# Kernel optimization log

Measured on AMD Instinct MI355X. Metric: run time of the kernel, lower is better.

The kernel has to match this reference:

```python
import jax, jax.numpy as jnp
import numpy as np

N = 50000      # nodes
E = 400000     # edges
G = 128        # graphs in batch
D_NODE = 64
EDGE_DIM = 72
HEADS = 4
H0, H1, H2 = 128, 128, 64
NC = 2
NEG = 0.2      # GATConv leaky_relu negative_slope default
D1 = H2 + EDGE_DIM - 1  # ffn input dim = 135


def _p(k, shape, s=0.1):
    return jax.random.normal(k, shape, dtype=jnp.float32) * s


def setup_inputs() -> dict:
    key = jax.random.key(0)
    ks = jax.random.split(key, 24)
    x = jax.random.normal(ks[0], (N, D_NODE), dtype=jnp.float32)
    edge_index = jax.random.randint(ks[1], (2, E), 0, N)
    edge_attr = jax.random.uniform(ks[2], (E, EDGE_DIM), dtype=jnp.float32)
    batch = jnp.sort(jax.random.randint(ks[3], (N,), 0, G))
    return dict(
        x=x, edge_index=edge_index, edge_attr=edge_attr, batch=batch,
        # GATConv layer 1: in=D_NODE, out=H0, heads=HEADS, concat
        W1=_p(ks[4], (D_NODE, HEADS * H0)), We1=_p(ks[5], (EDGE_DIM, HEADS * H0)),
        as1=_p(ks[6], (HEADS, H0)), ad1=_p(ks[7], (HEADS, H0)), ae1=_p(ks[8], (HEADS, H0)),
        b1=jnp.zeros((HEADS * H0,), jnp.float32),
        # GATConv layer 2: in=HEADS*H0, out=H1, heads=HEADS, concat
        W2=_p(ks[9], (HEADS * H0, HEADS * H1)), We2=_p(ks[10], (EDGE_DIM, HEADS * H1)),
        as2=_p(ks[11], (HEADS, H1)), ad2=_p(ks[12], (HEADS, H1)), ae2=_p(ks[13], (HEADS, H1)),
        b2=jnp.zeros((HEADS * H1,), jnp.float32),
        # GATConv layer 3: in=HEADS*H1, out=H2, heads=1, concat=False
        W3=_p(ks[14], (HEADS * H1, H2)), We3=_p(ks[15], (EDGE_DIM, H2)),
        as3=_p(ks[16], (1, H2)), ad3=_p(ks[17], (1, H2)), ae3=_p(ks[18], (1, H2)),
        b3=jnp.zeros((H2,), jnp.float32),
        # ffn: Linear(135 -> 67), ReLU, Linear(67 -> 2), Softmax
        Wf1=_p(ks[19], (D1, D1 // 2)), bf1=jnp.zeros((D1 // 2,), jnp.float32),
        Wf2=_p(ks[20], (D1 // 2, NC)), bf2=jnp.zeros((NC,), jnp.float32),
    )


def _seg_softmax(s, seg, n):
    # numerically-stable softmax over segments (per-destination neighborhoods)
    m = jax.ops.segment_max(s, seg, num_segments=n)
    m = jnp.where(jnp.isfinite(m), m, 0.0)
    e = jnp.exp(s - m[seg])
    z = jax.ops.segment_sum(e, seg, num_segments=n)
    return e / (z[seg] + 1e-16)


def _gat(x, src, dst, eattr, W, We, a_s, a_d, a_e, b, heads, oc, concat):
    # PyG GATConv with edge_dim: shared src/dst projection, edge feats only in attention
    n = x.shape[0]
    xs = (x @ W).reshape(n, heads, oc)            # [N,H,C]
    ee = (eattr @ We).reshape(-1, heads, oc)      # [Ea,H,C]
    alpha = (xs * a_s).sum(-1)[src] + (xs * a_d).sum(-1)[dst] + (ee * a_e).sum(-1)
    alpha = jax.nn.leaky_relu(alpha, NEG)         # [Ea,H]
    alpha = _seg_softmax(alpha, dst, n)
    out = jax.ops.segment_sum(xs[src] * alpha[:, :, None], dst, num_segments=n)
    out = out.reshape(n, heads * oc) if concat else out.mean(axis=1)
    return out + b


def reference(x, edge_index, edge_attr, batch,
              W1, We1, as1, ad1, ae1, b1,
              W2, We2, as2, ad2, ae2, b2,
              W3, We3, as3, ad3, ae3, b3,
              Wf1, bf1, Wf2, bf2):
    src, dst = edge_index[0], edge_index[1]
    n = x.shape[0]
    # --- 1-gram feature vector: scatter-add edge_attr[:, :-1] by graph of src ---
    eb = batch[src]
    og = jax.ops.segment_sum(edge_attr[:, :-1], eb, num_segments=G)   # [G, EDGE_DIM-1]
    og = og / jnp.maximum(jnp.linalg.norm(og, axis=1, keepdims=True), 1e-12)
    # --- add self loops, edge_attr fill_value='mean' (mean over incoming edges) ---
    ones_e = jnp.ones((src.shape[0],), x.dtype)
    deg = jax.ops.segment_sum(ones_e, dst, num_segments=n)
    loop_attr = jax.ops.segment_sum(edge_attr, dst, num_segments=n) / jnp.maximum(deg, 1.0)[:, None]
    nodes = jnp.arange(n)
    src_a = jnp.concatenate([src, nodes])
    dst_a = jnp.concatenate([dst, nodes])
    ea = jnp.concatenate([edge_attr, loop_attr], axis=0)
    # --- GAT stack with ReLU activations ---
    h = jax.nn.relu(_gat(x, src_a, dst_a, ea, W1, We1, as1, ad1, ae1, b1, HEADS, H0, True))
    h = jax.nn.relu(_gat(h, src_a, dst_a, ea, W2, We2, as2, ad2, ae2, b2, HEADS, H1, True))
    h = jax.nn.relu(_gat(h, src_a, dst_a, ea, W3, We3, as3, ad3, ae3, b3, 1, H2, False))
    # --- global mean pool over graphs ---
    cnt = jax.ops.segment_sum(jnp.ones((n,), x.dtype), batch, num_segments=G)
    pooled = jax.ops.segment_sum(h, batch, num_segments=G) / jnp.maximum(cnt, 1.0)[:, None]
    # --- concat + ffn (dropout p=0 in eval) + softmax ---
    z = jnp.concatenate([pooled, og], axis=1)                         # [G, 135]
    z = jax.nn.relu(z @ Wf1 + bf1)
    return jax.nn.softmax(z @ Wf2 + bf2, axis=1)
```

## Files before the change

kernel.cpp:

```cpp
#include <hip/hip_runtime.h>

#define NNODES 50000
#define NEDGES 400000
#define NEA    450000
#define NG     128
#define DEGCAP 96
#define OGW    72
#define NCH    49
#define PREPN  1128328
#define PREPB  4408
#define EDGEB  1563
#define OGB    (NG*16)

typedef unsigned short u16;
typedef unsigned int   u32;
typedef __attribute__((ext_vector_type(8))) short short8v;
typedef __attribute__((ext_vector_type(4))) float f32x4;

static inline int ceil_div(int a, int b){ return (a + b - 1)/b; }

__device__ __forceinline__ u16 f2bf(float f){
  u32 u = __builtin_bit_cast(u32, f);
  u = (u + 0x7fffu + ((u >> 16) & 1u)) >> 16;
  return (u16)u;
}
__device__ __forceinline__ float bfLO(u32 q){ return __builtin_bit_cast(float, q << 16); }
__device__ __forceinline__ float bfHI(u32 q){ return __builtin_bit_cast(float, q & 0xffff0000u); }
__device__ __forceinline__ void gload_lds16(const u16* g, u16* l){
  __builtin_amdgcn_global_load_lds((const __attribute__((address_space(1))) void*)g,
                                   (__attribute__((address_space(3))) void*)l, 16, 0, 0);
}

__global__ void k_prep_deg(const float* __restrict__ x, u16* __restrict__ xb,
                       const float* __restrict__ W1, u16* __restrict__ Wt1,
                       const float* __restrict__ W2, u16* __restrict__ Wt2,
                       const float* __restrict__ W3, u16* __restrict__ Wt3,
                       const float* __restrict__ We1, const float* __restrict__ ae1,
                       const float* __restrict__ We2, const float* __restrict__ ae2,
                       const float* __restrict__ We3, const float* __restrict__ ae3,
                       float* __restrict__ veall,
                       const int* __restrict__ src, const int* __restrict__ dst,
                       const int* __restrict__ batch,
                       int* __restrict__ deg, int* __restrict__ gb, int* __restrict__ gcnt){
  if (blockIdx.x >= PREPB){
    __shared__ int h[NG];
    int t = threadIdx.x;
    if (t < NG) h[t] = 0;
    __syncthreads();
    int e = (blockIdx.x - PREPB)*256 + t;
    if (e < NEDGES){
      atomicAdd(&deg[dst[e]], 1);
      int g = batch[src[e]];
      gb[e] = g;
      atomicAdd(&h[g], 1);
    }
    __syncthreads();
    if (t < NG && h[t]) atomicAdd(&gcnt[t], h[t]);
    return;
  }
  int i = blockIdx.x*blockDim.x + threadIdx.x;
  if (i < 800000){
    float4 v = ((const float4*)x)[i];
    ((ushort4*)xb)[i] = make_ushort4(f2bf(v.x), f2bf(v.y), f2bf(v.z), f2bf(v.w));
    return;
  }
  i -= 800000;
  if (i < 32768){
    int n = i >> 6, k = i & 63;
    Wt1[i] = f2bf(W1[(size_t)k*512 + n]);
    return;
  }
  i -= 32768;
  if (i < 262144){
    int n = i >> 9, k = i & 511;
    Wt2[i] = f2bf(W2[(size_t)k*512 + n]);
    return;
  }
  i -= 262144;
  if (i < 32768){
    int n = i >> 9, k = i & 511;
    Wt3[i] = f2bf(W3[(size_t)k*64 + n]);
    return;
  }
  i -= 32768;
  if (i < 648){
    const float* We; const float* ae; int H, C, basej, li;
    if (i < 288){ We = We1; ae = ae1; H = 4; C = 128; basej = 0; li = i; }
    else if (i < 576){ We = We2; ae = ae2; H = 4; C = 128; basej = 4; li = i - 288; }
    else { We = We3; ae = ae3; H = 1; C = 64; basej = 8; li = i - 576; }
    int k = li / H, h = li - k*H;
    const float* wrow = We + (size_t)k*H*C + (size_t)h*C;
    const float* arow = ae + (size_t)h*C;
    float s = 0.f;
    for (int c = 0; c < C; ++c) s += wrow[c]*arow[c];
    veall[k*9 + basej + h] = s;
  }
}

__global__ __launch_bounds__(1024) void k_chunksum(const int* __restrict__ deg, int* __restrict__ csum){
  __shared__ int s[1024];
  int t = threadIdx.x;
  int i = blockIdx.x*1024 + t;
  s[t] = (i < NNODES) ? deg[i]+1 : 0;
  __syncthreads();
  for (int o = 512; o > 0; o >>= 1){
    if (t < o) s[t] += s[t+o];
    __syncthreads();
  }
  if (t == 0) csum[blockIdx.x] = s[0];
}

__global__ __launch_bounds__(128) void k_scanmid(const int* __restrict__ csum, int* __restrict__ cbase,
                                                 const int* __restrict__ gcnt, int* __restrict__ goff,
                                                 int* __restrict__ gcur){
  __shared__ int sg[NG];
  int t = threadIdx.x;
  if (t < 64){
    int v0 = (t < NCH) ? csum[t] : 0;
    int v = v0;
    #pragma unroll
    for (int o = 1; o < 64; o <<= 1){
      int xsh = __shfl_up(v, o);
      if (t >= o) v += xsh;
    }
    if (t < NCH) cbase[t] = v - v0;
  }
  int vg = gcnt[t];
  sg[t] = vg;
  __syncthreads();
  for (int o = 1; o < NG; o <<= 1){
    int xg = (t >= o) ? sg[t-o] : 0;
    __syncthreads();
    sg[t] += xg;
    __syncthreads();
  }
  goff[t] = sg[t] - vg;
  gcur[t] = sg[t] - vg;
}

__global__ __launch_bounds__(1024) void k_scanout(const int* __restrict__ deg,
                                                  const int* __restrict__ cbase, int* __restrict__ off){
  __shared__ int s[1024];
  int t = threadIdx.x;
  int i = blockIdx.x*1024 + t;
  int v = (i < NNODES) ? deg[i]+1 : 0;
  s[t] = v;
  __syncthreads();
  for (int o = 1; o < 1024; o <<= 1){
    int xv = (t >= o) ? s[t-o] : 0;
    __syncthreads();
    s[t] += xv;
    __syncthreads();
  }
  if (i < NNODES){
    int incl = s[t] + cbase[blockIdx.x];
    off[i] = incl - v;
    if (i == NNODES-1) off[NNODES] = incl;
  }
}

__global__ void k_scatter(const int* __restrict__ src, const int* __restrict__ dst,
                          const int* __restrict__ gb, const int* __restrict__ off,
                          int* __restrict__ cnt, int* __restrict__ gcur,
                          int* __restrict__ csr_src, int* __restrict__ edgepos,
                          int* __restrict__ sortedeid){
  __shared__ int lcnt[NG];
  __shared__ int lbase[NG];
  int t = threadIdx.x;
  int e = blockIdx.x*256 + t;
  if (t < NG) lcnt[t] = 0;
  __syncthreads();
  int g = -1, lr = 0;
  if (e < NEDGES){
    int d = dst[e];
    int p = off[d] + atomicAdd(&cnt[d], 1);
    csr_src[p] = src[e];
    edgepos[e] = p;
    g = gb[e];
    lr = atomicAdd(&lcnt[g], 1);
  } else {
    int n2 = e - NEDGES;
    if (n2 < NNODES){
      int p = off[n2+1] - 1;
      csr_src[p] = n2;
    }
  }
  __syncthreads();
  if (t < NG && lcnt[t]) lbase[t] = atomicAdd(&gcur[t], lcnt[t]);
  __syncthreads();
  if (g >= 0) sortedeid[lbase[g] + lr] = e;
}

__global__ __launch_bounds__(256) void k_edge3(const float* __restrict__ attr,
    const int* __restrict__ goff, const int* __restrict__ gcnt,
    const int* __restrict__ sortedeid, const int* __restrict__ edgepos,
    const float* __restrict__ veall,
    float* __restrict__ se1, float* __restrict__ se2, float* __restrict__ se3,
    float* __restrict__ og){
  __shared__ float red[16][OGW];
  __shared__ float vel[72*9];
  int t = threadIdx.x;
  for (int i = t; i < 648; i += 256) vel[i] = veall[i];
  int g = blockIdx.x >> 4, chunk = blockIdx.x & 15;
  int lane = t & 63, w = t >> 6;
  int esub = lane >> 4, l16 = lane & 15;
  int slot = w*4 + esub;
  int beg = goff[g], cnt = gcnt[g];
  int cbeg = beg + ((cnt*chunk) >> 4);
  int cend = beg + ((cnt*(chunk+1)) >> 4);
  f32x4 acc  = {0.f,0.f,0.f,0.f};
  f32x4 acch = {0.f,0.f,0.f,0.f};
  __syncthreads();
  for (int i0 = cbeg; i0 < cend; i0 += 32){
    int p1 = i0 + slot, p2 = i0 + 16 + slot;
    int id1 = (p1 < cend) ? sortedeid[p1] : -1;
    int id2 = (p2 < cend) ? sortedeid[p2] : -1;
    int ep1 = (id1 >= 0) ? edgepos[id1] : 0;
    int ep2 = (id2 >= 0) ? edgepos[id2] : 0;
    f32x4 v1 = {0.f,0.f,0.f,0.f}, v2 = {0.f,0.f,0.f,0.f};
    f32x4 h1 = {0.f,0.f,0.f,0.f}, h2 = {0.f,0.f,0.f,0.f};
    if (id1 >= 0){
      v1 = *(const f32x4*)(attr + (size_t)id1*72 + l16*4);
      if (l16 < 2) h1 = *(const f32x4*)(attr + (size_t)id1*72 + 64 + l16*4);
    }
    if (id2 >= 0){
      v2 = *(const f32x4*)(attr + (size_t)id2*72 + l16*4);
      if (l16 < 2) h2 = *(const f32x4*)(attr + (size_t)id2*72 + 64 + l16*4);
    }
    acc += v1; acc += v2;
    if (l16 < 2){ acch += h1; acch += h2; }
    float s1[9], s2[9];
    int c0 = l16*4;
    #pragma unroll
    for (int j = 0; j < 9; ++j){
      s1[j] = v1[0]*vel[(c0+0)*9+j] + v1[1]*vel[(c0+1)*9+j]
            + v1[2]*vel[(c0+2)*9+j] + v1[3]*vel[(c0+3)*9+j];
      s2[j] = v2[0]*vel[(c0+0)*9+j] + v2[1]*vel[(c0+1)*9+j]
            + v2[2]*vel[(c0+2)*9+j] + v2[3]*vel[(c0+3)*9+j];
    }
    if (l16 < 2){
      int ct = 64 + l16*4;
      #pragma unroll
      for (int j = 0; j < 9; ++j){
        s1[j] += h1[0]*vel[(ct+0)*9+j] + h1[1]*vel[(ct+1)*9+j]
               + h1[2]*vel[(ct+2)*9+j] + h1[3]*vel[(ct+3)*9+j];
        s2[j] += h2[0]*vel[(ct+0)*9+j] + h2[1]*vel[(ct+1)*9+j]
               + h2[2]*vel[(ct+2)*9+j] + h2[3]*vel[(ct+3)*9+j];
      }
    }
    #pragma unroll
    for (int msk = 1; msk < 16; msk <<= 1){
      #pragma unroll
      for (int j = 0; j < 9; ++j){ s1[j] += __shfl_xor(s1[j], msk); s2[j] += __shfl_xor(s2[j], msk); }
    }
    if (l16 == 0 && id1 >= 0){
      *(float4*)(se1 + (size_t)ep1*4) = make_float4(s1[0], s1[1], s1[2], s1[3]);
      *(float4*)(se2 + (size_t)ep1*4) = make_float4(s1[4], s1[5], s1[6], s1[7]);
      se3[ep1] = s1[8];
    }
    if (l16 == 1 && id2 >= 0){
      *(float4*)(se1 + (size_t)ep2*4) = make_float4(s2[0], s2[1], s2[2], s2[3]);
      *(float4*)(se2 + (size_t)ep2*4) = make_float4(s2[4], s2[5], s2[6], s2[7]);
      se3[ep2] = s2[8];
    }
  }
  #pragma unroll
  for (int j = 0; j < 4; ++j) red[slot][l16*4 + j] = acc[j];
  if (l16 < 2){
    #pragma unroll
    for (int j = 0; j < 4; ++j) red[slot][64 + l16*4 + j] = acch[j];
  }
  __syncthreads();
  if (t < 71){
    float s = 0.f;
    #pragma unroll
    for (int q = 0; q < 16; ++q) s += red[q][t];
    atomicAdd(&og[g*OGW + t], s);
  }
}

__global__ __launch_bounds__(256) void k_gemm128(const u16* __restrict__ A,
    const u16* __restrict__ Bt, u16* __restrict__ C, int M, int K,
    const float* __restrict__ a_s, const float* __restrict__ a_d,
    float* __restrict__ ssrc, float* __restrict__ sdst){
  __shared__ __align__(16) u16 smem[128*128];
  u16* As = smem;
  u16* Bs = smem + 128*64;
  __shared__ float s_ps[128][2];
  __shared__ float s_pd[128][2];
  const int tid = threadIdx.x;
  const int wid = tid >> 6, lane = tid & 63;
  const int l15 = lane & 15, kslot = lane >> 4;
  const int wr = wid >> 1, wc = wid & 1;
  const int h = blockIdx.x;
  const int m0 = blockIdx.y * 128, n0 = h * 128;
  const int Nn = 512;
  f32x4 acc[4][4];
  #pragma unroll
  for (int mi = 0; mi < 4; ++mi)
    #pragma unroll
    for (int ni = 0; ni < 4; ++ni)
      acc[mi][ni] = (f32x4){0.f,0.f,0.f,0.f};

  for (int kt = 0; kt < K; kt += 64){
    #pragma unroll
    for (int r = 0; r < 4; ++r){
      int chunk = (r*4 + wid)*64 + lane;
      int row = chunk >> 3, c8 = chunk & 7;
      int srcc = c8 ^ (row & 7);
      int grow = m0 + row; if (grow > M-1) grow = M-1;
      gload_lds16(A + (size_t)grow*K + kt + srcc*8, &As[chunk*8]);
    }
    #pragma unroll
    for (int r = 0; r < 4; ++r){
      int chunk = (r*4 + wid)*64 + lane;
      int row = chunk >> 3, c8 = chunk & 7;
      int srcc = c8 ^ (row & 7);
      gload_lds16(Bt + (size_t)(n0+row)*K + kt + srcc*8, &Bs[chunk*8]);
    }
    __syncthreads();
    #pragma unroll
    for (int s = 0; s < 2; ++s){
      short8v a[4], b[4];
      #pragma unroll
      for (int mi = 0; mi < 4; ++mi){
        int row = wr*64 + mi*16 + l15;
        a[mi] = *(const short8v*)(&As[row*64 + (((s*4 + kslot) ^ (row&7))*8)]);
      }
      #pragma unroll
      for (int ni = 0; ni < 4; ++ni){
        int col = wc*64 + ni*16 + l15;
        b[ni] = *(const short8v*)(&Bs[col*64 + (((s*4 + kslot) ^ (col&7))*8)]);
      }
      #pragma unroll
      for (int mi = 0; mi < 4; ++mi)
        #pragma unroll
        for (int ni = 0; ni < 4; ++ni)
          acc[mi][ni] = __builtin_amdgcn_mfma_f32_16x16x32_bf16(a[mi], b[ni], acc[mi][ni], 0, 0, 0);
    }
    __syncthreads();
  }
  float asv[4], adv[4];
  #pragma unroll
  for (int ni = 0; ni < 4; ++ni){
    int c = wc*64 + ni*16 + l15;
    asv[ni] = a_s[h*128 + c];
    adv[ni] = a_d[h*128 + c];
  }
  #pragma unroll
  for (int mi = 0; mi < 4; ++mi){
    #pragma unroll
    for (int r = 0; r < 4; ++r){
      int row_l = wr*64 + mi*16 + kslot*4 + r;
      float ps = 0.f, pd = 0.f;
      #pragma unroll
      for (int ni = 0; ni < 4; ++ni){
        float v = acc[mi][ni][r];
        smem[row_l*128 + wc*64 + ni*16 + l15] = f2bf(v);
        ps += v*asv[ni];
        pd += v*adv[ni];
      }
      #pragma unroll
      for (int m = 8; m >= 1; m >>= 1){ ps += __shfl_xor(ps,m); pd += __shfl_xor(pd,m); }
      if (l15 == 0){ s_ps[row_l][wc] = ps; s_pd[row_l][wc] = pd; }
    }
  }
  __syncthreads();
  #pragma unroll
  for (int i = 0; i < 8; ++i){
    int c = i*256 + tid;
    int row = c >> 4, c16 = c & 15;
    int grow = m0 + row;
    if (grow < M)
      *(uint4*)(C + (size_t)grow*Nn + n0 + c16*8) = *(const uint4*)(&smem[row*128 + c16*8]);
  }
  if (tid < 128){
    int grow = m0 + tid;
    if (grow < M){
      ssrc[grow*4 + h] = s_ps[tid][0] + s_ps[tid][1];
      sdst[grow*4 + h] = s_pd[tid][0] + s_pd[tid][1];
    }
  }
}

__global__ __launch_bounds__(256) void k_gemm64(const u16* __restrict__ A,
    const u16* __restrict__ Bt, u16* __restrict__ C, int M,
    const float* __restrict__ a_s, const float* __restrict__ a_d,
    float* __restrict__ ssrc, float* __restrict__ sdst){
  __shared__ __align__(16) u16 As[64*64];
  __shared__ __align__(16) u16 Bs[64*64];
  const int tid = threadIdx.x;
  const int wid = tid >> 6, lane = tid & 63;
  const int l15 = lane & 15, kslot = lane >> 4;
  const int m0 = blockIdx.x * 64;
  f32x4 acc[4];
  #pragma unroll
  for (int ni = 0; ni < 4; ++ni) acc[ni] = (f32x4){0.f,0.f,0.f,0.f};
  for (int kt = 0; kt < 512; kt += 64){
    #pragma unroll
    for (int r = 0; r < 2; ++r){
      int chunk = r*256 + tid;
      int row = chunk >> 3, c8 = chunk & 7;
      int srcc = c8 ^ (row & 7);
      int grow = m0 + row; if (grow > M-1) grow = M-1;
      gload_lds16(A + (size_t)grow*512 + kt + srcc*8, &As[chunk*8]);
    }
    #pragma unroll
    for (int r = 0; r < 2; ++r){
      int chunk = r*256 + tid;
      int row = chunk >> 3, c8 = chunk & 7;
      int srcc = c8 ^ (row & 7);
      gload_lds16(Bt + (size_t)row*512 + kt + srcc*8, &Bs[chunk*8]);
    }
    __syncthreads();
    #pragma unroll
    for (int s = 0; s < 2; ++s){
      int row = wid*16 + l15;
      short8v a = *(const short8v*)(&As[row*64 + (((s*4 + kslot) ^ (row&7))*8)]);
      #pragma unroll
      for (int ni = 0; ni < 4; ++ni){
        int col = ni*16 + l15;
        short8v b = *(const short8v*)(&Bs[col*64 + (((s*4 + kslot) ^ (col&7))*8)]);
        acc[ni] = __builtin_amdgcn_mfma_f32_16x16x32_bf16(a, b, acc[ni], 0, 0, 0);
      }
    }
    __syncthreads();
  }
  #pragma unroll
  for (int r = 0; r < 4; ++r){
    int row_l = wid*16 + kslot*4 + r;
    int grow = m0 + row_l;
    float ps = 0.f, pd = 0.f;
    #pragma unroll
    for (int ni = 0; ni < 4; ++ni){
      float v = acc[ni][r];
      int c = ni*16 + l15;
      As[row_l*64 + c] = f2bf(v);
      ps += v*a_s[c];
      pd += v*a_d[c];
    }
    #pragma unroll
    for (int m = 8; m >= 1; m >>= 1){ ps += __shfl_xor(ps,m); pd += __shfl_xor(pd,m); }
    if (l15 == 0 && grow < M){ ssrc[grow] = ps; sdst[grow] = pd; }
  }
  __syncthreads();
  #pragma unroll
  for (int i = 0; i < 2; ++i){
    int c = i*256 + tid;
    int row = c >> 3, c8 = c & 7;
    int grow = m0 + row;
    if (grow < M)
      *(uint4*)(C + (size_t)grow*64 + c8*8) = *(const uint4*)(&As[row*64 + c8*8]);
  }
}

__global__ __launch_bounds__(256) void k_agg12(const u16* __restrict__ xs,
    const int* __restrict__ off, const int* __restrict__ csr_src,
    const float* __restrict__ ssrc, const float* __restrict__ sdst,
    const float* __restrict__ sep,
    const float* __restrict__ bias, u16* __restrict__ out){
  __shared__ float s_al[4][DEGCAP][4];
  __shared__ int   s_col[4][DEGCAP];
  int w = threadIdx.x >> 6, lane = threadIdx.x & 63;
  int n = blockIdx.x*4 + w;
  int beg = off[n];
  int deg = off[n+1] - beg;
  if (deg > DEGCAP) deg = DEGCAP;
  int es = lane >> 2, h = lane & 3;
  float sd = sdst[n*4+h];
  float sesum = 0.f;
  for (int e0 = 0; e0 < deg-1; e0 += 16){
    int e = e0 + es;
    if (e < deg-1){
      int col = csr_src[beg+e];
      float sr = sep[(size_t)(beg+e)*4 + h];
      sesum += sr;
      float s = ssrc[col*4+h] + sd + sr;
      s = (s > 0.f) ? s : 0.2f*s;
      s_al[w][e][h] = s;
      if (h == 0) s_col[w][e] = col;
    }
  }
  #pragma unroll
  for (int msk = 4; msk < 64; msk <<= 1) sesum += __shfl_xor(sesum, msk);
  if (es == 0){
    float slp = sesum / fmaxf((float)(deg-1), 1.0f);
    float s = ssrc[n*4+h] + sd + slp;
    s = (s > 0.f) ? s : 0.2f*s;
    s_al[w][deg-1][h] = s;
    if (h == 0) s_col[w][deg-1] = n;
  }
  float m = -1e30f;
  for (int e = es; e < deg; e += 16) m = fmaxf(m, s_al[w][e][h]);
  #pragma unroll
  for (int msk = 4; msk < 64; msk <<= 1) m = fmaxf(m, __shfl_xor(m, msk));
  float z = 0.f;
  for (int e = es; e < deg; e += 16){ float ex = __expf(s_al[w][e][h]-m); s_al[w][e][h] = ex; z += ex; }
  #pragma unroll
  for (int msk = 4; msk < 64; msk <<= 1) z += __shfl_xor(z, msk);
  float inv = 1.0f/(z + 1e-16f);
  for (int e = es; e < deg; e += 16) s_al[w][e][h] *= inv;
  int degR = (deg + 3) & ~3;
  for (int e = deg + es; e < degR; e += 16){ s_al[w][e][h] = 0.f; if (h == 0) s_col[w][e] = n; }
  __syncthreads();
  int hh = lane >> 4;
  f32x4 accA = {0.f,0.f,0.f,0.f}, accB = {0.f,0.f,0.f,0.f};
  for (int e = 0; e < degR; e += 4){
    int c0 = s_col[w][e+0], c1 = s_col[w][e+1], c2 = s_col[w][e+2], c3 = s_col[w][e+3];
    uint4 q0 = *(const uint4*)(xs + (size_t)c0*512 + lane*8);
    uint4 q1 = *(const uint4*)(xs + (size_t)c1*512 + lane*8);
    uint4 q2 = *(const uint4*)(xs + (size_t)c2*512 + lane*8);
    uint4 q3 = *(const uint4*)(xs + (size_t)c3*512 + lane*8);
    float a0 = s_al[w][e+0][hh], a1 = s_al[w][e+1][hh];
    float a2 = s_al[w][e+2][hh], a3 = s_al[w][e+3][hh];
    accA[0] += a0*bfLO(q0.x) + a1*bfLO(q1.x) + a2*bfLO(q2.x) + a3*bfLO(q3.x);
    accA[1] += a0*bfHI(q0.x) + a1*bfHI(q1.x) + a2*bfHI(q2.x) + a3*bfHI(q3.x);
    accA[2] += a0*bfLO(q0.y) + a1*bfLO(q1.y) + a2*bfLO(q2.y) + a3*bfLO(q3.y);
    accA[3] += a0*bfHI(q0.y) + a1*bfHI(q1.y) + a2*bfHI(q2.y) + a3*bfHI(q3.y);
    accB[0] += a0*bfLO(q0.z) + a1*bfLO(q1.z) + a2*bfLO(q2.z) + a3*bfLO(q3.z);
    accB[1] += a0*bfHI(q0.z) + a1*bfHI(q1.z) + a2*bfHI(q2.z) + a3*bfHI(q3.z);
    accB[2] += a0*bfLO(q0.w) + a1*bfLO(q1.w) + a2*bfLO(q2.w) + a3*bfLO(q3.w);
    accB[3] += a0*bfHI(q0.w) + a1*bfHI(q1.w) + a2*bfHI(q2.w) + a3*bfHI(q3.w);
  }
  f32x4 b0 = *(const f32x4*)(bias + lane*8);
  f32x4 b1 = *(const f32x4*)(bias + lane*8 + 4);
  short8v res;
  res[0] = (short)f2bf(fmaxf(accA[0]+b0[0], 0.f));
  res[1] = (short)f2bf(fmaxf(accA[1]+b0[1], 0.f));
  res[2] = (short)f2bf(fmaxf(accA[2]+b0[2], 0.f));
  res[3] = (short)f2bf(fmaxf(accA[3]+b0[3], 0.f));
  res[4] = (short)f2bf(fmaxf(accB[0]+b1[0], 0.f));
  res[5] = (short)f2bf(fmaxf(accB[1]+b1[1], 0.f));
  res[6] = (short)f2bf(fmaxf(accB[2]+b1[2], 0.f));
  res[7] = (short)f2bf(fmaxf(accB[3]+b1[3], 0.f));
  *(short8v*)(out + (size_t)n*512 + lane*8) = res;
}

__global__ __launch_bounds__(256) void k_agg3(const u16* __restrict__ xs,
    const int* __restrict__ off, const int* __restrict__ csr_src,
    const float* __restrict__ ssrc, const float* __restrict__ sdst,
    const float* __restrict__ se3,
    const float* __restrict__ bias, float* __restrict__ out){
  __shared__ float s_al[4][DEGCAP];
  __shared__ int   s_col[4][DEGCAP];
  int w = threadIdx.x >> 6, lane = threadIdx.x & 63;
  int n = blockIdx.x*4 + w;
  int beg = off[n];
  int deg = off[n+1] - beg;
  if (deg > DEGCAP) deg = DEGCAP;
  float sd = sdst[n];
  float sesum = 0.f;
  for (int e0 = 0; e0 < deg-1; e0 += 64){
    int e = e0 + lane;
    if (e < deg-1){
      int col = csr_src[beg+e];
      float sr = se3[beg+e];
      sesum += sr;
      float s = ssrc[col] + sd + sr;
      s = (s > 0.f) ? s : 0.2f*s;
      s_al[w][e] = s;
      s_col[w][e] = col;
    }
  }
  #pragma unroll
  for (int msk = 1; msk < 64; msk <<= 1) sesum += __shfl_xor(sesum, msk);
  if (lane == 0){
    float slp = sesum / fmaxf((float)(deg-1), 1.0f);
    float s = ssrc[n] + sd + slp;
    s = (s > 0.f) ? s : 0.2f*s;
    s_al[w][deg-1] = s;
    s_col[w][deg-1] = n;
  }
  float m = -1e30f;
  for (int e = lane; e < deg; e += 64) m = fmaxf(m, s_al[w][e]);
  #pragma unroll
  for (int msk = 1; msk < 64; msk <<= 1) m = fmaxf(m, __shfl_xor(m, msk));
  float z = 0.f;
  for (int e = lane; e < deg; e += 64){ float ex = __expf(s_al[w][e]-m); s_al[w][e] = ex; z += ex; }
  #pragma unroll
  for (int msk = 1; msk < 64; msk <<= 1) z += __shfl_xor(z, msk);
  float inv = 1.0f/(z + 1e-16f);
  for (int e = lane; e < deg; e += 64) s_al[w][e] *= inv;
  int degR = (deg + 3) & ~3;
  for (int e = deg + lane; e < degR; e += 64){ s_al[w][e] = 0.f; s_col[w][e] = n; }
  __syncthreads();
  int half = lane >> 5, cp = lane & 31;
  float a0 = 0.f, a1 = 0.f;
  for (int e = 0; e < degR; e += 4){
    int c0 = s_col[w][e + half], c1 = s_col[w][e + 2 + half];
    u32 q0 = *(const u32*)(xs + (size_t)c0*64 + cp*2);
    u32 q1 = *(const u32*)(xs + (size_t)c1*64 + cp*2);
    float al0 = s_al[w][e + half], al1 = s_al[w][e + 2 + half];
    a0 += al0*bfLO(q0) + al1*bfLO(q1);
    a1 += al0*bfHI(q0) + al1*bfHI(q1);
  }
  a0 += __shfl_xor(a0, 32);
  a1 += __shfl_xor(a1, 32);
  if (half == 0){
    float2 o;
    o.x = fmaxf(a0 + bias[cp*2+0], 0.f);
    o.y = fmaxf(a1 + bias[cp*2+1], 0.f);
    *(float2*)(out + (size_t)n*64 + cp*2) = o;
  }
}

__global__ __launch_bounds__(64) void k_pool(const float* __restrict__ h, const int* __restrict__ batch,
                                             float* __restrict__ pooled, int* __restrict__ cntg){
  int l = threadIdx.x;
  int start = blockIdx.x * 128;
  if (start >= NNODES) return;
  int endn = min(start + 128, NNODES);
  float acc = 0.f;
  int curg = batch[start];
  int run = 0;
  for (int n = start; n < endn; ++n){
    int g = batch[n];
    if (g != curg){
      atomicAdd(&pooled[curg*64+l], acc);
      if (l == 0) atomicAdd(&cntg[curg], run);
      acc = 0.f; run = 0; curg = g;
    }
    acc += h[(size_t)n*64 + l];
    ++run;
  }
  atomicAdd(&pooled[curg*64+l], acc);
  if (l == 0) atomicAdd(&cntg[curg], run);
}

__global__ void k_ffn(const float* __restrict__ pooled, const int* __restrict__ cntg,
                      const float* __restrict__ og,
                      const float* __restrict__ Wf1, const float* __restrict__ bf1,
                      const float* __restrict__ Wf2, const float* __restrict__ bf2,
                      float* __restrict__ out){
  __shared__ float z[135];
  __shared__ float z1[67];
  __shared__ float o2[2];
  int g = blockIdx.x, t = threadIdx.x;
  if (t < 64) z[t] = pooled[g*64+t] * (1.0f/fmaxf((float)cntg[g], 1.0f));
  else if (t < 135) z[t] = og[g*OGW + (t-64)];
  __syncthreads();
  if (t == 0){
    float s = 0.f;
    for (int k = 0; k < 71; ++k) s += z[64+k]*z[64+k];
    float scale = 1.0f / fmaxf(sqrtf(s), 1e-12f);
    for (int k = 0; k < 71; ++k) z[64+k] *= scale;
  }
  __syncthreads();
  if (t < 67){
    float s = bf1[t];
    for (int d = 0; d < 135; ++d) s += z[d]*Wf1[d*67+t];
    z1[t] = fmaxf(s, 0.f);
  }
  __syncthreads();
  if (t < 2){
    float s = bf2[t];
    for (int j = 0; j < 67; ++j) s += z1[j]*Wf2[j*2+t];
    o2[t] = s;
  }
  __syncthreads();
  if (t == 0){
    float m = fmaxf(o2[0], o2[1]);
    float e0 = expf(o2[0]-m), e1 = expf(o2[1]-m);
    float inv = 1.0f/(e0+e1);
    out[g*2+0] = e0*inv;
    out[g*2+1] = e1*inv;
  }
}

extern "C" void kernel_launch(void* const* d_in, const int* in_sizes, int n_in,
                              void* d_out, int out_size, void* d_ws, size_t ws_size,
                              hipStream_t stream){
  const float* x     = (const float*)d_in[0];
  const int*   ei    = (const int*)d_in[1];
  const float* eattr = (const float*)d_in[2];
  const int*   batch = (const int*)d_in[3];
  const float* W1  = (const float*)d_in[4];
  const float* We1 = (const float*)d_in[5];
  const float* as1 = (const float*)d_in[6];
  const float* ad1 = (const float*)d_in[7];
  const float* ae1 = (const float*)d_in[8];
  const float* b1  = (const float*)d_in[9];
  const float* W2  = (const float*)d_in[10];
  const float* We2 = (const float*)d_in[11];
  const float* as2 = (const float*)d_in[12];
  const float* ad2 = (const float*)d_in[13];
  const float* ae2 = (const float*)d_in[14];
  const float* b2  = (const float*)d_in[15];
  const float* W3  = (const float*)d_in[16];
  const float* We3 = (const float*)d_in[17];
  const float* as3 = (const float*)d_in[18];
  const float* ad3 = (const float*)d_in[19];
  const float* ae3 = (const float*)d_in[20];
  const float* b3  = (const float*)d_in[21];
  const float* Wf1 = (const float*)d_in[22];
  const float* bf1 = (const float*)d_in[23];
  const float* Wf2 = (const float*)d_in[24];
  const float* bf2 = (const float*)d_in[25];
  (void)in_sizes; (void)n_in; (void)out_size; (void)ws_size;
  const int* src = ei;
  const int* dst = ei + NEDGES;
  float* out = (float*)d_out;

  char* base = (char*)d_ws;
  size_t woff = 0;
  auto alloc = [&](size_t bytes)->char*{
    char* p = base + woff;
    woff += (bytes + 255) & ~(size_t)255;
    return p;
  };
  u16*   xsb    = (u16*)  alloc((size_t)NNODES*512*2);
  u16*   hb     = (u16*)  alloc((size_t)NNODES*512*2);
  u16*   xs3b   = (u16*)  alloc((size_t)NNODES*64*2);
  float* h3     = (float*)alloc((size_t)NNODES*64*4);
  u16*   xb     = (u16*)  alloc((size_t)NNODES*64*2);
  u16*   Wt1    = (u16*)  alloc((size_t)512*64*2);
  u16*   Wt2    = (u16*)  alloc((size_t)512*512*2);
  u16*   Wt3    = (u16*)  alloc((size_t)64*512*2);
  float* se1    = (float*)alloc((size_t)NEA*4*4);
  float* se2    = (float*)alloc((size_t)NEA*4*4);
  float* se3    = (float*)alloc((size_t)NEA*4);
  float* ssrc   = (float*)alloc((size_t)NNODES*4*4);
  float* sdst   = (float*)alloc((size_t)NNODES*4*4);
  float* veall  = (float*)alloc(72*9*4);
  int*   gb     = (int*)alloc((size_t)NEDGES*4);
  int*   csroff = (int*)alloc((size_t)(NNODES+1)*4);
  int*   csrsrc = (int*)alloc((size_t)NEA*4);
  int*   edgepos= (int*)alloc((size_t)NEDGES*4);
  int*   goff   = (int*)alloc(NG*4);
  int*   gcur   = (int*)alloc(NG*4);
  int*   sortedeid = (int*)alloc((size_t)NEDGES*4);
  int*   csum   = (int*)alloc(NCH*4);
  int*   cbase  = (int*)alloc(NCH*4);
  size_t z0 = woff;
  int*   deg    = (int*)alloc((size_t)NNODES*4);
  int*   cnt    = (int*)alloc((size_t)NNODES*4);
  int*   gcnt   = (int*)alloc(NG*4);
  float* og     = (float*)alloc((size_t)NG*OGW*4);
  float* pooled = (float*)alloc((size_t)NG*64*4);
  int*   cntg   = (int*)alloc((size_t)NG*4);
  size_t zlen = woff - z0;

  hipMemsetAsync(base + z0, 0, zlen, stream);

  k_prep_deg<<<PREPB + EDGEB,256,0,stream>>>(
      x, xb, W1, Wt1, W2, Wt2, W3, Wt3, We1, ae1, We2, ae2, We3, ae3, veall,
      src, dst, batch, deg, gb, gcnt);

  k_chunksum<<<NCH,1024,0,stream>>>(deg, csum);
  k_scanmid <<<1,128,0,stream>>>(csum, cbase, gcnt, goff, gcur);
  k_scanout <<<NCH,1024,0,stream>>>(deg, cbase, csroff);

  k_scatter<<<ceil_div(NEDGES+NNODES,256),256,0,stream>>>(src, dst, gb, csroff, cnt, gcur,
                                                          csrsrc, edgepos, sortedeid);

  k_edge3<<<OGB,256,0,stream>>>(eattr, goff, gcnt, sortedeid, edgepos, veall,
                                se1, se2, se3, og);

  dim3 g128(4, ceil_div(NNODES,128));

  k_gemm128<<<g128,256,0,stream>>>(xb, Wt1, xsb, NNODES, 64, as1, ad1, ssrc, sdst);
  k_agg12<<<NNODES/4,256,0,stream>>>(xsb, csroff, csrsrc, ssrc, sdst, se1, b1, hb);

  k_gemm128<<<g128,256,0,stream>>>(hb, Wt2, xsb, NNODES, 512, as2, ad2, ssrc, sdst);
  k_agg12<<<NNODES/4,256,0,stream>>>(xsb, csroff, csrsrc, ssrc, sdst, se2, b2, hb);

  k_gemm64<<<ceil_div(NNODES,64),256,0,stream>>>(hb, Wt3, xs3b, NNODES, as3, ad3, ssrc, sdst);
  k_agg3<<<NNODES/4,256,0,stream>>>(xs3b, csroff, csrsrc, ssrc, sdst, se3, b3, h3);

  k_pool<<<ceil_div(NNODES,128),64,0,stream>>>(h3, batch, pooled, cntg);
  k_ffn <<<NG,192,0,stream>>>(pooled, cntg, og, Wf1, bf1, Wf2, bf2, out);
}
```

Before: 518.3 us.

## Pack edge id with CSR position and process four edges per iteration in k_edge3

The scatter kernel now writes (edge id, CSR position) pairs into one sorted array, so k_edge3 no longer does a dependent random gather through edgepos. k_edge3 handles four edges per slot per iteration instead of two, putting more independent attribute loads in flight, and uses twice as many blocks per graph. This removes one indirect load chain per edge. In exchange it raises register pressure and doubles the number of og atomics.

```diff
diff --git a/kernel.cpp b/kernel.cpp
--- a/kernel.cpp
+++ b/kernel.cpp
@@ -10,7 +10,7 @@
 #define PREPN  1128328
 #define PREPB  4408
 #define EDGEB  1563
-#define OGB    (NG*16)
+#define OGB    (NG*32)
 
 typedef unsigned short u16;
 typedef unsigned int   u32;
@@ -162,106 +162,99 @@
 __global__ void k_scatter(const int* __restrict__ src, const int* __restrict__ dst,
                           const int* __restrict__ gb, const int* __restrict__ off,
                           int* __restrict__ cnt, int* __restrict__ gcur,
-                          int* __restrict__ csr_src, int* __restrict__ edgepos,
-                          int* __restrict__ sortedeid){
+                          int* __restrict__ csr_src, int2* __restrict__ sortedpair){
   __shared__ int lcnt[NG];
   __shared__ int lbase[NG];
   int t = threadIdx.x;
   int e = blockIdx.x*256 + t;
   if (t < NG) lcnt[t] = 0;
   __syncthreads();
-  int g = -1, lr = 0;
+  int g = -1, lr = 0, p = 0;
   if (e < NEDGES){
     int d = dst[e];
-    int p = off[d] + atomicAdd(&cnt[d], 1);
+    p = off[d] + atomicAdd(&cnt[d], 1);
     csr_src[p] = src[e];
-    edgepos[e] = p;
     g = gb[e];
     lr = atomicAdd(&lcnt[g], 1);
   } else {
     int n2 = e - NEDGES;
     if (n2 < NNODES){
-      int p = off[n2+1] - 1;
-      csr_src[p] = n2;
+      int q = off[n2+1] - 1;
+      csr_src[q] = n2;
     }
   }
   __syncthreads();
   if (t < NG && lcnt[t]) lbase[t] = atomicAdd(&gcur[t], lcnt[t]);
   __syncthreads();
-  if (g >= 0) sortedeid[lbase[g] + lr] = e;
+  if (g >= 0) sortedpair[lbase[g] + lr] = make_int2(e, p);
 }
 
 __global__ __launch_bounds__(256) void k_edge3(const float* __restrict__ attr,
     const int* __restrict__ goff, const int* __restrict__ gcnt,
-    const int* __restrict__ sortedeid, const int* __restrict__ edgepos,
-    const float* __restrict__ veall,
+    const int2* __restrict__ sortedpair, const float* __restrict__ veall,
     float* __restrict__ se1, float* __restrict__ se2, float* __restrict__ se3,
     float* __restrict__ og){
   __shared__ float red[16][OGW];
   __shared__ float vel[72*9];
   int t = threadIdx.x;
   for (int i = t; i < 648; i += 256) vel[i] = veall[i];
-  int g = blockIdx.x >> 4, chunk = blockIdx.x & 15;
+  int g = blockIdx.x >> 5, chunk = blockIdx.x & 31;
   int lane = t & 63, w = t >> 6;
   int esub = lane >> 4, l16 = lane & 15;
   int slot = w*4 + esub;
   int beg = goff[g], cnt = gcnt[g];
-  int cbeg = beg + ((cnt*chunk) >> 4);
-  int cend = beg + ((cnt*(chunk+1)) >> 4);
+  int cbeg = beg + ((cnt*chunk) >> 5);
+  int cend = beg + ((cnt*(chunk+1)) >> 5);
   f32x4 acc  = {0.f,0.f,0.f,0.f};
   f32x4 acch = {0.f,0.f,0.f,0.f};
   __syncthreads();
-  for (int i0 = cbeg; i0 < cend; i0 += 32){
-    int p1 = i0 + slot, p2 = i0 + 16 + slot;
-    int id1 = (p1 < cend) ? sortedeid[p1] : -1;
-    int id2 = (p2 < cend) ? sortedeid[p2] : -1;
-    int ep1 = (id1 >= 0) ? edgepos[id1] : 0;
-    int ep2 = (id2 >= 0) ? edgepos[id2] : 0;
-    f32x4 v1 = {0.f,0.f,0.f,0.f}, v2 = {0.f,0.f,0.f,0.f};
-    f32x4 h1 = {0.f,0.f,0.f,0.f}, h2 = {0.f,0.f,0.f,0.f};
-    if (id1 >= 0){
-      v1 = *(const f32x4*)(attr + (size_t)id1*72 + l16*4);
-      if (l16 < 2) h1 = *(const f32x4*)(attr + (size_t)id1*72 + 64 + l16*4);
-    }
-    if (id2 >= 0){
-      v2 = *(const f32x4*)(attr + (size_t)id2*72 + l16*4);
-      if (l16 < 2) h2 = *(const f32x4*)(attr + (size_t)id2*72 + 64 + l16*4);
-    }
-    acc += v1; acc += v2;
-    if (l16 < 2){ acch += h1; acch += h2; }
-    float s1[9], s2[9];
-    int c0 = l16*4;
-    #pragma unroll
-    for (int j = 0; j < 9; ++j){
-      s1[j] = v1[0]*vel[(c0+0)*9+j] + v1[1]*vel[(c0+1)*9+j]
-            + v1[2]*vel[(c0+2)*9+j] + v1[3]*vel[(c0+3)*9+j];
-      s2[j] = v2[0]*vel[(c0+0)*9+j] + v2[1]*vel[(c0+1)*9+j]
-            + v2[2]*vel[(c0+2)*9+j] + v2[3]*vel[(c0+3)*9+j];
-    }
-    if (l16 < 2){
-      int ct = 64 + l16*4;
+  for (int i0 = cbeg; i0 < cend; i0 += 64){
+    int2 pe[4];
+    #pragma unroll
+    for (int k = 0; k < 4; ++k){
+      int p = i0 + k*16 + slot;
+      pe[k] = (p < cend) ? sortedpair[p] : make_int2(-1, 0);
+    }
+    f32x4 v[4], vh[4];
+    #pragma unroll
+    for (int k = 0; k < 4; ++k){
+      v[k]  = (f32x4){0.f,0.f,0.f,0.f};
+      vh[k] = (f32x4){0.f,0.f,0.f,0.f};
+      if (pe[k].x >= 0){
+        v[k] = *(const f32x4*)(attr + (size_t)pe[k].x*72 + l16*4);
+        if (l16 < 2) vh[k] = *(const f32x4*)(attr + (size_t)pe[k].x*72 + 64 + l16*4);
+      }
+    }
+    #pragma unroll
+    for (int k = 0; k < 4; ++k){
+      acc += v[k];
+      if (l16 < 2) acch += vh[k];
+    }
+    int c0 = l16*4, ct = 64 + l16*4;
+    #pragma unroll
+    for (int k = 0; k < 4; ++k){
+      float s[9];
       #pragma unroll
-      for (int j = 0; j < 9; ++j){
-        s1[j] += h1[0]*vel[(ct+0)*9+j] + h1[1]*vel[(ct+1)*9+j]
-               + h1[2]*vel[(ct+2)*9+j] + h1[3]*vel[(ct+3)*9+j];
-        s2[j] += h2[0]*vel[(ct+0)*9+j] + h2[1]*vel[(ct+1)*9+j]
-               + h2[2]*vel[(ct+2)*9+j] + h2[3]*vel[(ct+3)*9+j];
+      for (int j = 0; j < 9; ++j)
+        s[j] = v[k][0]*vel[(c0+0)*9+j] + v[k][1]*vel[(c0+1)*9+j]
+             + v[k][2]*vel[(c0+2)*9+j] + v[k][3]*vel[(c0+3)*9+j];
+      if (l16 < 2){
+        #pragma unroll
+        for (int j = 0; j < 9; ++j)
+          s[j] += vh[k][0]*vel[(ct+0)*9+j] + vh[k][1]*vel[(ct+1)*9+j]
+                + vh[k][2]*vel[(ct+2)*9+j] + vh[k][3]*vel[(ct+3)*9+j];
       }
-    }
-    #pragma unroll
-    for (int msk = 1; msk < 16; msk <<= 1){
       #pragma unroll
-      for (int j = 0; j < 9; ++j){ s1[j] += __shfl_xor(s1[j], msk); s2[j] += __shfl_xor(s2[j], msk); }
-    }
-    if (l16 == 0 && id1 >= 0){
-      *(float4*)(se1 + (size_t)ep1*4) = make_float4(s1[0], s1[1], s1[2], s1[3]);
-      *(float4*)(se2 + (size_t)ep1*4) = make_float4(s1[4], s1[5], s1[6], s1[7]);
-      se3[ep1] = s1[8];
-    }
-    if (l16 == 1 && id2 >= 0){
-      *(float4*)(se1 + (size_t)ep2*4) = make_float4(s2[0], s2[1], s2[2], s2[3]);
-      *(float4*)(se2 + (size_t)ep2*4) = make_float4(s2[4], s2[5], s2[6], s2[7]);
-      se3[ep2] = s2[8];
+      for (int msk = 1; msk < 16; msk <<= 1){
+        #pragma unroll
+        for (int j = 0; j < 9; ++j) s[j] += __shfl_xor(s[j], msk);
+      }
+      if (l16 == k && pe[k].x >= 0){
+        int p = pe[k].y;
+        *(float4*)(se1 + (size_t)p*4) = make_float4(s[0], s[1], s[2], s[3]);
+        *(float4*)(se2 + (size_t)p*4) = make_float4(s[4], s[5], s[6], s[7]);
+        se3[p] = s[8];
+      }
     }
   }
   #pragma unroll
@@ -725,10 +718,9 @@
   int*   gb     = (int*)alloc((size_t)NEDGES*4);
   int*   csroff = (int*)alloc((size_t)(NNODES+1)*4);
   int*   csrsrc = (int*)alloc((size_t)NEA*4);
-  int*   edgepos= (int*)alloc((size_t)NEDGES*4);
+  int2*  sortedpair = (int2*)alloc((size_t)NEDGES*8);
   int*   goff   = (int*)alloc(NG*4);
   int*   gcur   = (int*)alloc(NG*4);
-  int*   sortedeid = (int*)alloc((size_t)NEDGES*4);
   int*   csum   = (int*)alloc(NCH*4);
   int*   cbase  = (int*)alloc(NCH*4);
   size_t z0 = woff;
@@ -751,10 +743,9 @@
   k_scanout <<<NCH,1024,0,stream>>>(deg, cbase, csroff);
 
   k_scatter<<<ceil_div(NEDGES+NNODES,256),256,0,stream>>>(src, dst, gb, csroff, cnt, gcur,
-                                                          csrsrc, edgepos, sortedeid);
-
-  k_edge3<<<OGB,256,0,stream>>>(eattr, goff, gcnt, sortedeid, edgepos, veall,
-                                se1, se2, se3, og);
+                                                          csrsrc, sortedpair);
+
+  k_edge3<<<OGB,256,0,stream>>>(eattr, goff, gcnt, sortedpair, veall, se1, se2, se3, og);
 
   dim3 g128(4, ceil_div(NNODES,128));
 
```

Result: slower. 535.6 us (+3.3%).
